# Optimization experiments

Hardware: AMD Instinct MI355X
Metric: run time of the kernel (lower is better)

The kernel has to match this reference:

```python
import jax, jax.numpy as jnp
import numpy as np

N, E, IN_C, HID, OUT_C = 50000, 800000, 128, 32, 32
EPS_BN = 1e-5


def gat_layer(x, src, dst, W, a_src, a_dst, bias, heads, out_c, concat):
    n = x.shape[0]
    h = (x @ W).reshape(n, heads, out_c)                    # [N,H,C]
    al_src = jnp.sum(h * a_src, axis=-1)                    # [N,H]
    al_dst = jnp.sum(h * a_dst, axis=-1)                    # [N,H]
    e = jax.nn.leaky_relu(al_src[src] + al_dst[dst], 0.2)   # [Etot,H]
    # segment softmax over incoming edges of each dst node
    m = jax.ops.segment_max(e, dst, num_segments=n)
    e = jnp.exp(e - jax.lax.stop_gradient(m)[dst])
    s = jax.ops.segment_sum(e, dst, num_segments=n)
    alpha = e / (s[dst] + 1e-16)                            # [Etot,H]
    msg = h[src] * alpha[..., None]                         # [Etot,H,C]
    out = jax.ops.segment_sum(msg, dst, num_segments=n)     # [N,H,C]
    out = out.reshape(n, heads * out_c) if concat else out.mean(axis=1)
    return out + bias


def bn_eval(x, w, b, m, v):
    return (x - m) * (w * jax.lax.rsqrt(v + EPS_BN)) + b


def setup_inputs() -> dict:
    key = jax.random.key(0)
    ks = jax.random.split(key, 12)
    f32 = jnp.float32
    inp = {
        'x': jax.random.normal(ks[0], (N, IN_C), dtype=f32),
        'edge_index': jax.random.randint(ks[1], (2, E), 0, N, dtype=jnp.int64),
        'w1': jax.random.normal(ks[2], (IN_C, 4 * HID), dtype=f32) * 0.1,
        'as1': jax.random.normal(ks[3], (4, HID), dtype=f32) * 0.1,
        'ad1': jax.random.normal(ks[4], (4, HID), dtype=f32) * 0.1,
        'b1': jnp.zeros((4 * HID,), f32),
        'bn1_w': jnp.ones((4 * HID,), f32), 'bn1_b': jnp.zeros((4 * HID,), f32),
        'bn1_m': jnp.zeros((4 * HID,), f32), 'bn1_v': jnp.ones((4 * HID,), f32),
        'w2': jax.random.normal(ks[5], (4 * HID, 4 * HID), dtype=f32) * 0.1,
        'as2': jax.random.normal(ks[6], (4, HID), dtype=f32) * 0.1,
        'ad2': jax.random.normal(ks[7], (4, HID), dtype=f32) * 0.1,
        'b2': jnp.zeros((4 * HID,), f32),
        'bn2_w': jnp.ones((4 * HID,), f32), 'bn2_b': jnp.zeros((4 * HID,), f32),
        'bn2_m': jnp.zeros((4 * HID,), f32), 'bn2_v': jnp.ones((4 * HID,), f32),
        'w3': jax.random.normal(ks[8], (4 * HID, OUT_C), dtype=f32) * 0.1,
        'as3': jax.random.normal(ks[9], (1, OUT_C), dtype=f32) * 0.1,
        'ad3': jax.random.normal(ks[10], (1, OUT_C), dtype=f32) * 0.1,
        'b3': jnp.zeros((OUT_C,), f32),
    }
    return inp


def reference(x, edge_index, w1, as1, ad1, b1, bn1_w, bn1_b, bn1_m, bn1_v,
              w2, as2, ad2, b2, bn2_w, bn2_b, bn2_m, bn2_v,
              w3, as3, ad3, b3):
    n = x.shape[0]
    loop = jnp.arange(n, dtype=edge_index.dtype)
    src = jnp.concatenate([edge_index[0], loop])  # add_self_loops (PyG default)
    dst = jnp.concatenate([edge_index[1], loop])
    # layer 1: GAT(heads=4, concat) -> BN(eval) -> relu (dropout=eval identity)
    h = gat_layer(x, src, dst, w1, as1, ad1, b1, 4, HID, True)
    h = jax.nn.relu(bn_eval(h, bn1_w, bn1_b, bn1_m, bn1_v))
    # layer 2
    h = gat_layer(h, src, dst, w2, as2, ad2, b2, 4, HID, True)
    h = jax.nn.relu(bn_eval(h, bn2_w, bn2_b, bn2_m, bn2_v))
    # layer 3: heads=1, concat=False
    return gat_layer(h, src, dst, w3, as3, ad3, b3, 1, OUT_C, False)
```

## Files before the change

### kernel.cpp

```cpp
#include <hip/hip_runtime.h>
#include <hip/hip_fp16.h>
#include <cstdint>


#define NBCHUNK 128
#define MAXBK 512

typedef _Float16 f16x8 __attribute__((ext_vector_type(8)));
typedef float f32x4 __attribute__((ext_vector_type(4)));

__device__ __forceinline__ float lrelu02(float x) {
  return x > 0.f ? x : 0.2f * x;
}

__device__ __forceinline__ float expw(float x) {
  return __expf(fminf(x, 80.f));
}

__global__ void detect_kernel(const unsigned* __restrict__ ei, int* __restrict__ flag) {
  int lane = threadIdx.x;
  unsigned w = ei[2 * lane + 1];
  unsigned long long nz = __ballot(w != 0u);
  if (lane == 0) *flag = (nz == 0ull) ? 1 : 0;
}

__global__ __launch_bounds__(256) void bcount_kernel(const void* __restrict__ ei, int E,
                                                     const int* __restrict__ flag,
                                                     int* __restrict__ counts,
                                                     int nbk, int chunk) {
  __shared__ int hist[MAXBK];
  for (int i = threadIdx.x; i < nbk; i += 256) hist[i] = 0;
  __syncthreads();
  int lo = blockIdx.x * chunk;
  int hi = lo + chunk; if (hi > E) hi = E;
  const bool is64 = (*flag) != 0;
  for (int e = lo + threadIdx.x; e < hi; e += 256) {
    int d = is64 ? (int)((const long long*)ei)[(size_t)E + e] : ((const int*)ei)[E + e];
    atomicAdd(&hist[d >> 7], 1);
  }
  __syncthreads();
  for (int i = threadIdx.x; i < nbk; i += 256)
    counts[(size_t)blockIdx.x * nbk + i] = hist[i];
}

__global__ void bscanT_kernel(int* __restrict__ counts, int* __restrict__ T, int nbk) {
  int b = blockIdx.x;
  int t = threadIdx.x;
  int lane = t & 63;
  int v = counts[(size_t)t * nbk + b];
  int inc = v;
#pragma unroll
  for (int off = 1; off < 64; off <<= 1) {
    int u = __shfl_up(inc, off);
    if (lane >= off) inc += u;
  }
  __shared__ int w0;
  if (t == 63) w0 = inc;
  __syncthreads();
  int wb = (t >= 64) ? w0 : 0;
  counts[(size_t)t * nbk + b] = wb + inc - v;
  if (t == 127) T[b] = wb + inc;
}

__global__ void bscanE_kernel(const int* __restrict__ T, int* __restrict__ EB, int nbk) {
  int lane = threadIdx.x;
  int carry = 0;
  for (int start = 0; start < nbk; start += 64) {
    int i = start + lane;
    int v = (i < nbk) ? T[i] : 0;
    int inc = v;
#pragma unroll
    for (int off = 1; off < 64; off <<= 1) {
      int u = __shfl_up(inc, off);
      if (lane >= off) inc += u;
    }
    if (i < nbk) EB[i] = inc - v + carry;
    carry += __shfl(inc, 63);
  }
  if (lane == 0) EB[nbk] = carry;
}

__global__ __launch_bounds__(256) void bemit_kernel(const void* __restrict__ ei, int E,
                                                    const int* __restrict__ flag,
                                                    const int* __restrict__ counts,
                                                    const int* __restrict__ EB,
                                                    int nbk, int chunk,
                                                    unsigned* __restrict__ binned) {
  __shared__ int cur[MAXBK];
  for (int i = threadIdx.x; i < nbk; i += 256)
    cur[i] = counts[(size_t)blockIdx.x * nbk + i] + EB[i];
  __syncthreads();
  int lo = blockIdx.x * chunk;
  int hi = lo + chunk; if (hi > E) hi = E;
  const bool is64 = (*flag) != 0;
  for (int e = lo + threadIdx.x; e < hi; e += 256) {
    int s, d;
    if (is64) {
      const long long* p = (const long long*)ei;
      s = (int)p[e];
      d = (int)p[(size_t)E + e];
    } else {
      const int* p = (const int*)ei;
      s = p[e];
      d = p[E + e];
    }
    int pos = atomicAdd(&cur[d >> 7], 1);
    binned[pos] = ((unsigned)(d & 127) << 16) | (unsigned)s;
  }
}

__global__ __launch_bounds__(256) void bscatter2_kernel(const unsigned* __restrict__ binned,
                                                        const int* __restrict__ EB,
                                                        int* __restrict__ row_ptr,
                                                        int* __restrict__ csr_src,
                                                        int n, int E) {
  __shared__ int hist[128];
  __shared__ int cur[128];
  __shared__ int w0s;
  const int b = blockIdx.x;
  const int t = threadIdx.x;
  const int bb = b << 7;
  if (t < 128) hist[t] = 0;
  __syncthreads();
  const int lo = EB[b], hi = EB[b + 1];
  for (int i = lo + t; i < hi; i += 256)
    atomicAdd(&hist[binned[i] >> 16], 1);
  __syncthreads();
  int lane = t & 63;
  int v = (t < 128) ? hist[t] : 0;
  int inc = v;
#pragma unroll
  for (int off = 1; off < 64; off <<= 1) {
    int u = __shfl_up(inc, off);
    if (lane >= off) inc += u;
  }
  if (t == 63) w0s = inc;
  __syncthreads();
  int exc = ((t >= 64 && t < 128) ? w0s : 0) + inc - v;
  if (t < 128 && bb + t < n) {
    int rp = EB[b] + bb + t + exc;
    row_ptr[bb + t] = rp;
    csr_src[rp] = bb + t;
    cur[t] = rp + 1;
  }
  if (b == 0 && t == 0) row_ptr[n] = E + n;
  __syncthreads();
  for (int i = lo + t; i < hi; i += 256) {
    unsigned pv = binned[i];
    int pos = atomicAdd(&cur[pv >> 16], 1);
    csr_src[pos] = (int)(pv & 0xFFFFu);
  }
}

__global__ void wcvt_kernel(const float* __restrict__ W, _Float16* __restrict__ Wt,
                            int OUTC) {
  int idx = blockIdx.x * 256 + threadIdx.x;
  if (idx >= 128 * OUTC) return;
  int k = idx / OUTC, c = idx % OUTC;
  Wt[(size_t)c * 128 + k] = (_Float16)W[idx];
}

template <int OUTC, int H, typename AT>
__global__ __launch_bounds__(256) void mfma_gemm_al_kernel(
    const AT* __restrict__ A, const _Float16* __restrict__ Wt,
    const float* __restrict__ a_src, const float* __restrict__ a_dst,
    __half* __restrict__ Hout, float* __restrict__ alS, float* __restrict__ alD,
    int n) {
  constexpr int NT = OUTC / 16;
  constexpr int APH = 136;

  __shared__ __align__(16) _Float16 A_lds[64 * APH];
  __shared__ __align__(16) _Float16 W_lds[OUTC * APH];

  const int t = threadIdx.x;
  const int r0 = blockIdx.x * 64;

  if constexpr (sizeof(AT) == 4) {
#pragma unroll
    for (int i = 0; i < 8; ++i) {
      int slot = t + i * 256;
      int r = slot >> 5, q = slot & 31;
      float4 v = make_float4(0.f, 0.f, 0.f, 0.f);
      if (r0 + r < n) v = *(const float4*)((const float*)A + (size_t)(r0 + r) * 128 + q * 4);
      __half2 p0 = __floats2half2_rn(v.x, v.y);
      __half2 p1 = __floats2half2_rn(v.z, v.w);
      uint2 pk;
      pk.x = *(unsigned*)&p0;
      pk.y = *(unsigned*)&p1;
      *(uint2*)&A_lds[r * APH + q * 4] = pk;
    }
  } else {
#pragma unroll
    for (int i = 0; i < 4; ++i) {
      int slot = t + i * 256;
      int r = slot >> 4, q = slot & 15;
      uint4 raw = make_uint4(0u, 0u, 0u, 0u);
      if (r0 + r < n) raw = *(const uint4*)((const __half*)A + (size_t)(r0 + r) * 128 + q * 8);
      *(uint4*)&A_lds[r * APH + q * 8] = raw;
    }
  }
#pragma unroll
  for (int i = 0; i < OUTC / 16; ++i) {
    int slot = t + i * 256;
    int c = slot >> 4, q = slot & 15;
    uint4 raw = *(const uint4*)(Wt + (size_t)c * 128 + q * 8);
    *(uint4*)&W_lds[c * APH + q * 8] = raw;
  }
  __syncthreads();

  const int w = t >> 6;
  const int lane = t & 63;
  const int lrow = lane & 15;
  const int lk = lane >> 4;

  f32x4 acc[NT];
#pragma unroll
  for (int i = 0; i < NT; ++i) acc[i] = (f32x4){0.f, 0.f, 0.f, 0.f};

#pragma unroll
  for (int kc = 0; kc < 4; ++kc) {
    f16x8 a = *(const f16x8*)&A_lds[(w * 16 + lrow) * APH + kc * 32 + lk * 8];
#pragma unroll
    for (int ct = 0; ct < NT; ++ct) {
      f16x8 b = *(const f16x8*)&W_lds[(ct * 16 + lrow) * APH + kc * 32 + lk * 8];
      acc[ct] = __builtin_amdgcn_mfma_f32_16x16x32_f16(a, b, acc[ct], 0, 0, 0);
    }
  }

  const int rbase = r0 + w * 16 + lk * 4;
#pragma unroll
  for (int ct = 0; ct < NT; ++ct) {
#pragma unroll
    for (int j = 0; j < 4; ++j) {
      int r = rbase + j;
      if (r < n) Hout[(size_t)r * OUTC + ct * 16 + lrow] = __float2half(acc[ct][j]);
    }
  }

#pragma unroll
  for (int h = 0; h < H; ++h) {
    float as0 = a_src[h * 32 + lrow], as1 = a_src[h * 32 + 16 + lrow];
    float ad0 = a_dst[h * 32 + lrow], ad1 = a_dst[h * 32 + 16 + lrow];
#pragma unroll
    for (int j = 0; j < 4; ++j) {
      float ps = acc[2 * h][j] * as0 + acc[2 * h + 1][j] * as1;
      float pd = acc[2 * h][j] * ad0 + acc[2 * h + 1][j] * ad1;
#pragma unroll
      for (int off = 1; off < 16; off <<= 1) {
        ps += __shfl_xor(ps, off);
        pd += __shfl_xor(pd, off);
      }
      if (lrow == 0) {
        int r = rbase + j;
        if (r < n) {
          alS[(size_t)r * H + h] = ps;
          alD[(size_t)r * H + h] = pd;
        }
      }
    }
  }
}

template <int H, bool BN, typename OutT>
__global__ __launch_bounds__(256) void agg_kernel(
    const int* __restrict__ row_ptr, const int* __restrict__ csr_src,
    const float* __restrict__ alS, const float* __restrict__ alD,
    const __half* __restrict__ hfeat, const float* __restrict__ bias,
    const float* __restrict__ bnw, const float* __restrict__ bnb,
    const float* __restrict__ bnm, const float* __restrict__ bnv,
    OutT* __restrict__ out, int n) {
  constexpr int LPN = (H == 4) ? 64 : 32;
  constexpr int NPB = 256 / LPN;
  constexpr int KCAP = 96;
  constexpr int RSH = (H == 4) ? 8 : 6;

  __shared__ __align__(16) float sW[NPB][KCAP * H];
  __shared__ int sOff[NPB][KCAP];

  const int slot = threadIdx.x / LPN;
  const int sl = threadIdx.x % LPN;
  const int v = blockIdx.x * NPB + slot;
  const bool active = v < n;
  const char* hb = (const char*)hfeat;

  int rs = 0, re = 0;
  if (active) { rs = row_ptr[v]; re = row_ptr[v + 1]; }
  const int deg = re - rs;
  const int degS = deg < KCAP ? deg : KCAP;

  if constexpr (H == 4) {
    float4 ad4 = make_float4(0.f, 0.f, 0.f, 0.f);
    if (active) ad4 = *(const float4*)(alD + (size_t)v * 4);
    float den0 = 0.f, den1 = 0.f, den2 = 0.f, den3 = 0.f;
    for (int k = sl; k < degS; k += 64) {
      int s = csr_src[rs + k];
      sOff[slot][k] = s << RSH;
      float4 a4 = *(const float4*)(alS + (size_t)s * 4);
      float u0 = expw(lrelu02(a4.x + ad4.x));
      float u1 = expw(lrelu02(a4.y + ad4.y));
      float u2 = expw(lrelu02(a4.z + ad4.z));
      float u3 = expw(lrelu02(a4.w + ad4.w));
      ((float4*)&sW[slot][0])[k] = make_float4(u0, u1, u2, u3);
      den0 += u0; den1 += u1; den2 += u2; den3 += u3;
    }
#pragma unroll
    for (int off = 32; off >= 1; off >>= 1) {
      den0 += __shfl_xor(den0, off);
      den1 += __shfl_xor(den1, off);
      den2 += __shfl_xor(den2, off);
      den3 += __shfl_xor(den3, off);
    }

    const int c = 2 * sl;
    const int h = sl >> 4;
    const unsigned cb2 = (unsigned)(c * 2);
    float2 acc = make_float2(0.f, 0.f);
    int j = 0;
    for (; j + 4 <= degS; j += 4) {
      unsigned o0 = (unsigned)sOff[slot][j + 0] + cb2;
      unsigned o1 = (unsigned)sOff[slot][j + 1] + cb2;
      unsigned o2 = (unsigned)sOff[slot][j + 2] + cb2;
      unsigned o3 = (unsigned)sOff[slot][j + 3] + cb2;
      float w0 = sW[slot][(j + 0) * 4 + h];
      float w1 = sW[slot][(j + 1) * 4 + h];
      float w2 = sW[slot][(j + 2) * 4 + h];
      float w3 = sW[slot][(j + 3) * 4 + h];
      float2 f0 = __half22float2(*(const __half2*)(hb + o0));
      float2 f1 = __half22float2(*(const __half2*)(hb + o1));
      float2 f2 = __half22float2(*(const __half2*)(hb + o2));
      float2 f3 = __half22float2(*(const __half2*)(hb + o3));
      acc.x = fmaf(w0, f0.x, acc.x); acc.y = fmaf(w0, f0.y, acc.y);
      acc.x = fmaf(w1, f1.x, acc.x); acc.y = fmaf(w1, f1.y, acc.y);
      acc.x = fmaf(w2, f2.x, acc.x); acc.y = fmaf(w2, f2.y, acc.y);
      acc.x = fmaf(w3, f3.x, acc.x); acc.y = fmaf(w3, f3.y, acc.y);
    }
    for (; j < degS; ++j) {
      unsigned o = (unsigned)sOff[slot][j] + cb2;
      float w = sW[slot][j * 4 + h];
      float2 f = __half22float2(*(const __half2*)(hb + o));
      acc.x = fmaf(w, f.x, acc.x); acc.y = fmaf(w, f.y, acc.y);
    }
    float den = (h == 0) ? den0 : (h == 1) ? den1 : (h == 2) ? den2 : den3;
    if (deg > KCAP) {
      float adh = alD[(size_t)v * 4 + h];
      for (int e = rs + KCAP; e < re; ++e) {
        int s = csr_src[e];
        float u = expw(lrelu02(alS[(size_t)s * 4 + h] + adh));
        den += u;
        float2 f = __half22float2(*(const __half2*)(hb + ((unsigned)(s << RSH) + cb2)));
        acc.x = fmaf(u, f.x, acc.x); acc.y = fmaf(u, f.y, acc.y);
      }
    }
    if (active) {
      float inv = 1.f / (den + 1e-16f);
      float2 b2v = *(const float2*)(bias + c);
      float g0 = acc.x * inv + b2v.x;
      float g1 = acc.y * inv + b2v.y;
      if constexpr (BN) {
        float2 bw = *(const float2*)(bnw + c);
        float2 bb = *(const float2*)(bnb + c);
        float2 bm = *(const float2*)(bnm + c);
        float2 bv = *(const float2*)(bnv + c);
        g0 = (g0 - bm.x) * (bw.x * rsqrtf(bv.x + 1e-5f)) + bb.x;
        g1 = (g1 - bm.y) * (bw.y * rsqrtf(bv.y + 1e-5f)) + bb.y;
        g0 = fmaxf(g0, 0.f);
        g1 = fmaxf(g1, 0.f);
      }
      if constexpr (sizeof(OutT) == 2) {
        __half2 o2 = __floats2half2_rn(g0, g1);
        *(__half2*)((__half*)out + (size_t)v * 128 + c) = o2;
      } else {
        *(float2*)((float*)out + (size_t)v * 128 + c) = make_float2(g0, g1);
      }
    }
  } else {
    float ad = active ? alD[v] : 0.f;
    float den = 0.f;
    for (int k = sl; k < degS; k += 32) {
      int s = csr_src[rs + k];
      sOff[slot][k] = s << RSH;
      float u = expw(lrelu02(alS[s] + ad));
      sW[slot][k] = u;
      den += u;
    }
#pragma unroll
    for (int off = 16; off >= 1; off >>= 1) den += __shfl_xor(den, off);

    const int c = sl;
    const unsigned cb2 = (unsigned)(c * 2);
    float acc = 0.f;
    int j = 0;
    for (; j + 4 <= degS; j += 4) {
      unsigned o0 = (unsigned)sOff[slot][j + 0] + cb2;
      unsigned o1 = (unsigned)sOff[slot][j + 1] + cb2;
      unsigned o2 = (unsigned)sOff[slot][j + 2] + cb2;
      unsigned o3 = (unsigned)sOff[slot][j + 3] + cb2;
      float w0 = sW[slot][j + 0], w1 = sW[slot][j + 1];
      float w2 = sW[slot][j + 2], w3 = sW[slot][j + 3];
      float f0 = __half2float(*(const __half*)(hb + o0));
      float f1 = __half2float(*(const __half*)(hb + o1));
      float f2 = __half2float(*(const __half*)(hb + o2));
      float f3 = __half2float(*(const __half*)(hb + o3));
      acc = fmaf(w0, f0, acc); acc = fmaf(w1, f1, acc);
      acc = fmaf(w2, f2, acc); acc = fmaf(w3, f3, acc);
    }
    for (; j < degS; ++j) {
      unsigned o = (unsigned)sOff[slot][j] + cb2;
      float w = sW[slot][j];
      acc = fmaf(w, __half2float(*(const __half*)(hb + o)), acc);
    }
    if (deg > KCAP) {
      for (int e = rs + KCAP; e < re; ++e) {
        int s = csr_src[e];
        float u = expw(lrelu02(alS[s] + ad));
        den += u;
        acc = fmaf(u, __half2float(*(const __half*)(hb + ((unsigned)(s << RSH) + cb2))), acc);
      }
    }
    if (active) {
      ((float*)out)[(size_t)v * 32 + c] = acc / (den + 1e-16f) + bias[c];
    }
  }
}

extern "C" void kernel_launch(void* const* d_in, const int* in_sizes, int n_in,
                              void* d_out, int out_size, void* d_ws, size_t ws_size,
                              hipStream_t stream) {
  const float* x = (const float*)d_in[0];
  const void* ei = d_in[1];
  const float* w1 = (const float*)d_in[2];
  const float* as1 = (const float*)d_in[3];
  const float* ad1 = (const float*)d_in[4];
  const float* b1 = (const float*)d_in[5];
  const float* bn1w = (const float*)d_in[6];
  const float* bn1b = (const float*)d_in[7];
  const float* bn1m = (const float*)d_in[8];
  const float* bn1v = (const float*)d_in[9];
  const float* w2 = (const float*)d_in[10];
  const float* as2 = (const float*)d_in[11];
  const float* ad2 = (const float*)d_in[12];
  const float* b2 = (const float*)d_in[13];
  const float* bn2w = (const float*)d_in[14];
  const float* bn2b = (const float*)d_in[15];
  const float* bn2m = (const float*)d_in[16];
  const float* bn2v = (const float*)d_in[17];
  const float* w3 = (const float*)d_in[18];
  const float* as3 = (const float*)d_in[19];
  const float* ad3 = (const float*)d_in[20];
  const float* b3 = (const float*)d_in[21];

  const int N = in_sizes[0] / 128;
  const int E = in_sizes[1] / 2;
  const int nbk = (N + 127) / 128;
  const int chunk = (E + NBCHUNK - 1) / NBCHUNK;

  char* base = (char*)d_ws;
  size_t off = 0;
  auto alloc = [&](size_t bytes) {
    void* p = base + off;
    off = (off + bytes + 255) & ~(size_t)255;
    return p;
  };
  int* flag = (int*)alloc(4);
  int* counts = (int*)alloc((size_t)NBCHUNK * nbk * 4);
  int* T = (int*)alloc((size_t)nbk * 4);
  int* EB = (int*)alloc((size_t)(nbk + 1) * 4);
  unsigned* binned = (unsigned*)alloc((size_t)E * 4);
  int* row_ptr = (int*)alloc((size_t)(N + 1) * 4);
  int* csr_src = (int*)alloc((size_t)(E + N) * 4);
  _Float16* Wt16 = (_Float16*)alloc((size_t)128 * 128 * 2);
  __half* hbuf = (__half*)alloc((size_t)N * 128 * 2);
  __half* gbuf = (__half*)alloc((size_t)N * 128 * 2);
  float* alS = (float*)alloc((size_t)N * 4 * 4);
  float* alD = (float*)alloc((size_t)N * 4 * 4);
  (void)ws_size;

  detect_kernel<<<1, 64, 0, stream>>>((const unsigned*)ei, flag);
  bcount_kernel<<<NBCHUNK, 256, 0, stream>>>(ei, E, flag, counts, nbk, chunk);
  bscanT_kernel<<<nbk, NBCHUNK, 0, stream>>>(counts, T, nbk);
  bscanE_kernel<<<1, 64, 0, stream>>>(T, EB, nbk);
  bemit_kernel<<<NBCHUNK, 256, 0, stream>>>(ei, E, flag, counts, EB, nbk, chunk, binned);
  bscatter2_kernel<<<nbk, 256, 0, stream>>>(binned, EB, row_ptr, csr_src, N, E);

  const int rowBlocks = (N + 63) / 64;

  wcvt_kernel<<<(128 * 128 + 255) / 256, 256, 0, stream>>>(w1, Wt16, 128);
  mfma_gemm_al_kernel<128, 4, float><<<rowBlocks, 256, 0, stream>>>(
      x, Wt16, as1, ad1, hbuf, alS, alD, N);
  agg_kernel<4, true, __half><<<(N + 3) / 4, 256, 0, stream>>>(
      row_ptr, csr_src, alS, alD, hbuf, b1, bn1w, bn1b, bn1m, bn1v, gbuf, N);
  wcvt_kernel<<<(128 * 128 + 255) / 256, 256, 0, stream>>>(w2, Wt16, 128);
  mfma_gemm_al_kernel<128, 4, __half><<<rowBlocks, 256, 0, stream>>>(
      gbuf, Wt16, as2, ad2, hbuf, alS, alD, N);
  agg_kernel<4, true, __half><<<(N + 3) / 4, 256, 0, stream>>>(
      row_ptr, csr_src, alS, alD, hbuf, b2, bn2w, bn2b, bn2m, bn2v, gbuf, N);
  wcvt_kernel<<<(128 * 32 + 255) / 256, 256, 0, stream>>>(w3, Wt16, 32);
  mfma_gemm_al_kernel<32, 1, __half><<<rowBlocks, 256, 0, stream>>>(
      gbuf, Wt16, as3, ad3, hbuf, alS, alD, N);
  agg_kernel<1, false, float><<<(N + 7) / 8, 256, 0, stream>>>(
      row_ptr, csr_src, alS, alD, hbuf, b3, nullptr, nullptr, nullptr, nullptr,
      (float*)d_out, N);
}
```

Baseline: 199.2 us.

## Widen aggregation gathers by splitting edges across half-waves, merge launch setup kernels

```diff
diff --git a/kernel.cpp b/kernel.cpp
--- a/kernel.cpp
+++ b/kernel.cpp
@@ -17,23 +17,24 @@
   return __expf(fminf(x, 80.f));
 }
 
-__global__ void detect_kernel(const unsigned* __restrict__ ei, int* __restrict__ flag) {
-  int lane = threadIdx.x;
-  unsigned w = ei[2 * lane + 1];
-  unsigned long long nz = __ballot(w != 0u);
-  if (lane == 0) *flag = (nz == 0ull) ? 1 : 0;
+__device__ __forceinline__ int detect64(const unsigned* ei) {
+  int is64 = 1;
+  for (int i = 1; i < 128; i += 2)
+    if (ei[i] != 0u) { is64 = 0; break; }
+  return is64;
 }
 
 __global__ __launch_bounds__(256) void bcount_kernel(const void* __restrict__ ei, int E,
-                                                     const int* __restrict__ flag,
                                                      int* __restrict__ counts,
                                                      int nbk, int chunk) {
   __shared__ int hist[MAXBK];
+  __shared__ int sIs64;
   for (int i = threadIdx.x; i < nbk; i += 256) hist[i] = 0;
+  if (threadIdx.x == 0) sIs64 = detect64((const unsigned*)ei);
   __syncthreads();
   int lo = blockIdx.x * chunk;
   int hi = lo + chunk; if (hi > E) hi = E;
-  const bool is64 = (*flag) != 0;
+  const bool is64 = sIs64 != 0;
   for (int e = lo + threadIdx.x; e < hi; e += 256) {
     int d = is64 ? (int)((const long long*)ei)[(size_t)E + e] : ((const int*)ei)[E + e];
     atomicAdd(&hist[d >> 7], 1);
@@ -81,18 +82,19 @@
 }
 
 __global__ __launch_bounds__(256) void bemit_kernel(const void* __restrict__ ei, int E,
-                                                    const int* __restrict__ flag,
                                                     const int* __restrict__ counts,
                                                     const int* __restrict__ EB,
                                                     int nbk, int chunk,
                                                     unsigned* __restrict__ binned) {
   __shared__ int cur[MAXBK];
+  __shared__ int sIs64;
   for (int i = threadIdx.x; i < nbk; i += 256)
     cur[i] = counts[(size_t)blockIdx.x * nbk + i] + EB[i];
+  if (threadIdx.x == 0) sIs64 = detect64((const unsigned*)ei);
   __syncthreads();
   int lo = blockIdx.x * chunk;
   int hi = lo + chunk; if (hi > E) hi = E;
-  const bool is64 = (*flag) != 0;
+  const bool is64 = sIs64 != 0;
   for (int e = lo + threadIdx.x; e < hi; e += 256) {
     int s, d;
     if (is64) {
@@ -152,12 +154,23 @@
   }
 }
 
-__global__ void wcvt_kernel(const float* __restrict__ W, _Float16* __restrict__ Wt,
-                            int OUTC) {
+__global__ void wcvt_all_kernel(const float* __restrict__ W1, const float* __restrict__ W2,
+                                const float* __restrict__ W3,
+                                _Float16* __restrict__ Wt1, _Float16* __restrict__ Wt2,
+                                _Float16* __restrict__ Wt3) {
   int idx = blockIdx.x * 256 + threadIdx.x;
-  if (idx >= 128 * OUTC) return;
-  int k = idx / OUTC, c = idx % OUTC;
-  Wt[(size_t)c * 128 + k] = (_Float16)W[idx];
+  if (idx < 16384) {
+    int k = idx >> 7, c = idx & 127;
+    Wt1[(size_t)c * 128 + k] = (_Float16)W1[idx];
+  } else if (idx < 32768) {
+    int i = idx - 16384;
+    int k = i >> 7, c = i & 127;
+    Wt2[(size_t)c * 128 + k] = (_Float16)W2[i];
+  } else if (idx < 36864) {
+    int i = idx - 32768;
+    int k = i >> 5, c = i & 31;
+    Wt3[(size_t)c * 128 + k] = (_Float16)W3[i];
+  }
 }
 
 template <int OUTC, int H, typename AT>
@@ -311,66 +324,114 @@
       den3 += __shfl_xor(den3, off);
     }
 
-    const int c = 2 * sl;
-    const int h = sl >> 4;
+    const int half = sl >> 5;
+    const int l5 = sl & 31;
+    const int c = l5 * 4;
+    const int h = l5 >> 3;
     const unsigned cb2 = (unsigned)(c * 2);
-    float2 acc = make_float2(0.f, 0.f);
+    float a0 = 0.f, a1 = 0.f, a2 = 0.f, a3 = 0.f;
     int j = 0;
-    for (; j + 4 <= degS; j += 4) {
-      unsigned o0 = (unsigned)sOff[slot][j + 0] + cb2;
-      unsigned o1 = (unsigned)sOff[slot][j + 1] + cb2;
-      unsigned o2 = (unsigned)sOff[slot][j + 2] + cb2;
-      unsigned o3 = (unsigned)sOff[slot][j + 3] + cb2;
-      float w0 = sW[slot][(j + 0) * 4 + h];
-      float w1 = sW[slot][(j + 1) * 4 + h];
-      float w2 = sW[slot][(j + 2) * 4 + h];
-      float w3 = sW[slot][(j + 3) * 4 + h];
-      float2 f0 = __half22float2(*(const __half2*)(hb + o0));
-      float2 f1 = __half22float2(*(const __half2*)(hb + o1));
-      float2 f2 = __half22float2(*(const __half2*)(hb + o2));
-      float2 f3 = __half22float2(*(const __half2*)(hb + o3));
-      acc.x = fmaf(w0, f0.x, acc.x); acc.y = fmaf(w0, f0.y, acc.y);
-      acc.x = fmaf(w1, f1.x, acc.x); acc.y = fmaf(w1, f1.y, acc.y);
-      acc.x = fmaf(w2, f2.x, acc.x); acc.y = fmaf(w2, f2.y, acc.y);
-      acc.x = fmaf(w3, f3.x, acc.x); acc.y = fmaf(w3, f3.y, acc.y);
-    }
-    for (; j < degS; ++j) {
-      unsigned o = (unsigned)sOff[slot][j] + cb2;
-      float w = sW[slot][j * 4 + h];
-      float2 f = __half22float2(*(const __half2*)(hb + o));
-      acc.x = fmaf(w, f.x, acc.x); acc.y = fmaf(w, f.y, acc.y);
-    }
+    for (; j + 8 <= degS; j += 8) {
+      int e0 = j + half, e1 = j + 2 + half, e2 = j + 4 + half, e3 = j + 6 + half;
+      unsigned o0 = (unsigned)sOff[slot][e0] + cb2;
+      unsigned o1 = (unsigned)sOff[slot][e1] + cb2;
+      unsigned o2 = (unsigned)sOff[slot][e2] + cb2;
+      unsigned o3 = (unsigned)sOff[slot][e3] + cb2;
+      float w0 = sW[slot][e0 * 4 + h], w1 = sW[slot][e1 * 4 + h];
+      float w2 = sW[slot][e2 * 4 + h], w3 = sW[slot][e3 * 4 + h];
+      uint2 r0v = *(const uint2*)(hb + o0);
+      uint2 r1v = *(const uint2*)(hb + o1);
+      uint2 r2v = *(const uint2*)(hb + o2);
+      uint2 r3v = *(const uint2*)(hb + o3);
+      float2 f0l = __half22float2(*(const __half2*)&r0v.x);
+      float2 f0h = __half22float2(*(const __half2*)&r0v.y);
+      float2 f1l = __half22float2(*(const __half2*)&r1v.x);
+      float2 f1h = __half22float2(*(const __half2*)&r1v.y);
+      float2 f2l = __half22float2(*(const __half2*)&r2v.x);
+      float2 f2h = __half22float2(*(const __half2*)&r2v.y);
+      float2 f3l = __half22float2(*(const __half2*)&r3v.x);
+      float2 f3h = __half22float2(*(const __half2*)&r3v.y);
+      a0 = fmaf(w0, f0l.x, a0); a1 = fmaf(w0, f0l.y, a1);
+      a2 = fmaf(w0, f0h.x, a2); a3 = fmaf(w0, f0h.y, a3);
+      a0 = fmaf(w1, f1l.x, a0); a1 = fmaf(w1, f1l.y, a1);
+      a2 = fmaf(w1, f1h.x, a2); a3 = fmaf(w1, f1h.y, a3);
+      a0 = fmaf(w2, f2l.x, a0); a1 = fmaf(w2, f2l.y, a1);
+      a2 = fmaf(w2, f2h.x, a2); a3 = fmaf(w2, f2h.y, a3);
+      a0 = fmaf(w3, f3l.x, a0); a1 = fmaf(w3, f3l.y, a1);
+      a2 = fmaf(w3, f3h.x, a2); a3 = fmaf(w3, f3h.y, a3);
+    }
+    for (; j + 2 <= degS; j += 2) {
+      int e = j + half;
+      unsigned o = (unsigned)sOff[slot][e] + cb2;
+      float w = sW[slot][e * 4 + h];
+      uint2 rv = *(const uint2*)(hb + o);
+      float2 fl = __half22float2(*(const __half2*)&rv.x);
+      float2 fh = __half22float2(*(const __half2*)&rv.y);
+      a0 = fmaf(w, fl.x, a0); a1 = fmaf(w, fl.y, a1);
+      a2 = fmaf(w, fh.x, a2); a3 = fmaf(w, fh.y, a3);
+    }
+    if ((degS & 1) && half == 0) {
+      int e = degS - 1;
+      unsigned o = (unsigned)sOff[slot][e] + cb2;
+      float w = sW[slot][e * 4 + h];
+      uint2 rv = *(const uint2*)(hb + o);
+      float2 fl = __half22float2(*(const __half2*)&rv.x);
+      float2 fh = __half22float2(*(const __half2*)&rv.y);
+      a0 = fmaf(w, fl.x, a0); a1 = fmaf(w, fl.y, a1);
+      a2 = fmaf(w, fh.x, a2); a3 = fmaf(w, fh.y, a3);
+    }
+    a0 += __shfl_xor(a0, 32);
+    a1 += __shfl_xor(a1, 32);
+    a2 += __shfl_xor(a2, 32);
+    a3 += __shfl_xor(a3, 32);
+
     float den = (h == 0) ? den0 : (h == 1) ? den1 : (h == 2) ? den2 : den3;
     if (deg > KCAP) {
       float adh = alD[(size_t)v * 4 + h];
-      for (int e = rs + KCAP; e < re; ++e) {
-        int s = csr_src[e];
-        float u = expw(lrelu02(alS[(size_t)s * 4 + h] + adh));
-        den += u;
-        float2 f = __half22float2(*(const __half2*)(hb + ((unsigned)(s << RSH) + cb2)));
-        acc.x = fmaf(u, f.x, acc.x); acc.y = fmaf(u, f.y, acc.y);
+      if (half == 0) {
+        for (int e = rs + KCAP; e < re; ++e) {
+          int s = csr_src[e];
+          float u = expw(lrelu02(alS[(size_t)s * 4 + h] + adh));
+          den += u;
+          uint2 rv = *(const uint2*)(hb + ((unsigned)(s << RSH) + cb2));
+          float2 fl = __half22float2(*(const __half2*)&rv.x);
+          float2 fh = __half22float2(*(const __half2*)&rv.y);
+          a0 = fmaf(u, fl.x, a0); a1 = fmaf(u, fl.y, a1);
+          a2 = fmaf(u, fh.x, a2); a3 = fmaf(u, fh.y, a3);
+        }
+      } else {
+        for (int e = rs + KCAP; e < re; ++e) {
+          int s = csr_src[e];
+          den += expw(lrelu02(alS[(size_t)s * 4 + h] + adh));
+        }
       }
     }
-    if (active) {
+    if (active && half == 0) {
       float inv = 1.f / (den + 1e-16f);
-      float2 b2v = *(const float2*)(bias + c);
-      float g0 = acc.x * inv + b2v.x;
-      float g1 = acc.y * inv + b2v.y;
+      float4 b4 = *(const float4*)(bias + c);
+      float g0 = a0 * inv + b4.x;
+      float g1 = a1 * inv + b4.y;
+      float g2 = a2 * inv + b4.z;
+      float g3 = a3 * inv + b4.w;
       if constexpr (BN) {
-        float2 bw = *(const float2*)(bnw + c);
-        float2 bb = *(const float2*)(bnb + c);
-        float2 bm = *(const float2*)(bnm + c);
-        float2 bv = *(const float2*)(bnv + c);
-        g0 = (g0 - bm.x) * (bw.x * rsqrtf(bv.x + 1e-5f)) + bb.x;
-        g1 = (g1 - bm.y) * (bw.y * rsqrtf(bv.y + 1e-5f)) + bb.y;
-        g0 = fmaxf(g0, 0.f);
-        g1 = fmaxf(g1, 0.f);
+        float4 bw = *(const float4*)(bnw + c);
+        float4 bb = *(const float4*)(bnb + c);
+        float4 bm = *(const float4*)(bnm + c);
+        float4 bv = *(const float4*)(bnv + c);
+        g0 = fmaxf((g0 - bm.x) * (bw.x * rsqrtf(bv.x + 1e-5f)) + bb.x, 0.f);
+        g1 = fmaxf((g1 - bm.y) * (bw.y * rsqrtf(bv.y + 1e-5f)) + bb.y, 0.f);
+        g2 = fmaxf((g2 - bm.z) * (bw.z * rsqrtf(bv.z + 1e-5f)) + bb.z, 0.f);
+        g3 = fmaxf((g3 - bm.w) * (bw.w * rsqrtf(bv.w + 1e-5f)) + bb.w, 0.f);
       }
       if constexpr (sizeof(OutT) == 2) {
-        __half2 o2 = __floats2half2_rn(g0, g1);
-        *(__half2*)((__half*)out + (size_t)v * 128 + c) = o2;
+        __half2 p0 = __floats2half2_rn(g0, g1);
+        __half2 p1 = __floats2half2_rn(g2, g3);
+        uint2 pk;
+        pk.x = *(unsigned*)&p0;
+        pk.y = *(unsigned*)&p1;
+        *(uint2*)((__half*)out + (size_t)v * 128 + c) = pk;
       } else {
-        *(float2*)((float*)out + (size_t)v * 128 + c) = make_float2(g0, g1);
+        *(float4*)((float*)out + (size_t)v * 128 + c) = make_float4(g0, g1, g2, g3);
       }
     }
   } else {
@@ -386,39 +447,58 @@
 #pragma unroll
     for (int off = 16; off >= 1; off >>= 1) den += __shfl_xor(den, off);
 
-    const int c = sl;
-    const unsigned cb2 = (unsigned)(c * 2);
-    float acc = 0.f;
+    const int quad = sl >> 4;
+    const int l4 = sl & 15;
+    const int c2 = l4 * 2;
+    const unsigned cb2 = (unsigned)(c2 * 2);
+    float a0 = 0.f, a1 = 0.f;
     int j = 0;
     for (; j + 4 <= degS; j += 4) {
-      unsigned o0 = (unsigned)sOff[slot][j + 0] + cb2;
-      unsigned o1 = (unsigned)sOff[slot][j + 1] + cb2;
-      unsigned o2 = (unsigned)sOff[slot][j + 2] + cb2;
-      unsigned o3 = (unsigned)sOff[slot][j + 3] + cb2;
-      float w0 = sW[slot][j + 0], w1 = sW[slot][j + 1];
-      float w2 = sW[slot][j + 2], w3 = sW[slot][j + 3];
-      float f0 = __half2float(*(const __half*)(hb + o0));
-      float f1 = __half2float(*(const __half*)(hb + o1));
-      float f2 = __half2float(*(const __half*)(hb + o2));
-      float f3 = __half2float(*(const __half*)(hb + o3));
-      acc = fmaf(w0, f0, acc); acc = fmaf(w1, f1, acc);
-      acc = fmaf(w2, f2, acc); acc = fmaf(w3, f3, acc);
-    }
-    for (; j < degS; ++j) {
-      unsigned o = (unsigned)sOff[slot][j] + cb2;
-      float w = sW[slot][j];
-      acc = fmaf(w, __half2float(*(const __half*)(hb + o)), acc);
-    }
+      int e0 = j + quad, e1 = j + 2 + quad;
+      unsigned o0 = (unsigned)sOff[slot][e0] + cb2;
+      unsigned o1 = (unsigned)sOff[slot][e1] + cb2;
+      float w0 = sW[slot][e0], w1 = sW[slot][e1];
+      float2 f0 = __half22float2(*(const __half2*)(hb + o0));
+      float2 f1 = __half22float2(*(const __half2*)(hb + o1));
+      a0 = fmaf(w0, f0.x, a0); a1 = fmaf(w0, f0.y, a1);
+      a0 = fmaf(w1, f1.x, a0); a1 = fmaf(w1, f1.y, a1);
+    }
+    for (; j + 2 <= degS; j += 2) {
+      int e = j + quad;
+      unsigned o = (unsigned)sOff[slot][e] + cb2;
+      float w = sW[slot][e];
+      float2 f = __half22float2(*(const __half2*)(hb + o));
+      a0 = fmaf(w, f.x, a0); a1 = fmaf(w, f.y, a1);
+    }
+    if ((degS & 1) && quad == 0) {
+      int e = degS - 1;
+      unsigned o = (unsigned)sOff[slot][e] + cb2;
+      float w = sW[slot][e];
+      float2 f = __half22float2(*(const __half2*)(hb + o));
+      a0 = fmaf(w, f.x, a0); a1 = fmaf(w, f.y, a1);
+    }
+    a0 += __shfl_xor(a0, 16);
+    a1 += __shfl_xor(a1, 16);
+
     if (deg > KCAP) {
-      for (int e = rs + KCAP; e < re; ++e) {
-        int s = csr_src[e];
-        float u = expw(lrelu02(alS[s] + ad));
-        den += u;
-        acc = fmaf(u, __half2float(*(const __half*)(hb + ((unsigned)(s << RSH) + cb2))), acc);
+      if (quad == 0) {
+        for (int e = rs + KCAP; e < re; ++e) {
+          int s = csr_src[e];
+          float u = expw(lrelu02(alS[s] + ad));
+          den += u;
+          float2 f = __half22float2(*(const __half2*)(hb + ((unsigned)(s << RSH) + cb2)));
+          a0 = fmaf(u, f.x, a0); a1 = fmaf(u, f.y, a1);
+        }
+      } else {
+        for (int e = rs + KCAP; e < re; ++e)
+          den += expw(lrelu02(alS[csr_src[e]] + ad));
       }
     }
-    if (active) {
-      ((float*)out)[(size_t)v * 32 + c] = acc / (den + 1e-16f) + bias[c];
+    if (active && quad == 0) {
+      float inv = 1.f / (den + 1e-16f);
+      float2 b2v = *(const float2*)(bias + c2);
+      ((float2*)((float*)out + (size_t)v * 32))[l4] =
+          make_float2(a0 * inv + b2v.x, a1 * inv + b2v.y);
     }
   }
 }
@@ -461,42 +541,40 @@
     off = (off + bytes + 255) & ~(size_t)255;
     return p;
   };
-  int* flag = (int*)alloc(4);
   int* counts = (int*)alloc((size_t)NBCHUNK * nbk * 4);
   int* T = (int*)alloc((size_t)nbk * 4);
   int* EB = (int*)alloc((size_t)(nbk + 1) * 4);
   unsigned* binned = (unsigned*)alloc((size_t)E * 4);
   int* row_ptr = (int*)alloc((size_t)(N + 1) * 4);
   int* csr_src = (int*)alloc((size_t)(E + N) * 4);
-  _Float16* Wt16 = (_Float16*)alloc((size_t)128 * 128 * 2);
+  _Float16* Wt1 = (_Float16*)alloc((size_t)128 * 128 * 2);
+  _Float16* Wt2 = (_Float16*)alloc((size_t)128 * 128 * 2);
+  _Float16* Wt3 = (_Float16*)alloc((size_t)32 * 128 * 2);
   __half* hbuf = (__half*)alloc((size_t)N * 128 * 2);
   __half* gbuf = (__half*)alloc((size_t)N * 128 * 2);
   float* alS = (float*)alloc((size_t)N * 4 * 4);
   float* alD = (float*)alloc((size_t)N * 4 * 4);
   (void)ws_size;
 
-  detect_kernel<<<1, 64, 0, stream>>>((const unsigned*)ei, flag);
-  bcount_kernel<<<NBCHUNK, 256, 0, stream>>>(ei, E, flag, counts, nbk, chunk);
+  wcvt_all_kernel<<<144, 256, 0, stream>>>(w1, w2, w3, Wt1, Wt2, Wt3);
+  bcount_kernel<<<NBCHUNK, 256, 0, stream>>>(ei, E, counts, nbk, chunk);
   bscanT_kernel<<<nbk, NBCHUNK, 0, stream>>>(counts, T, nbk);
   bscanE_kernel<<<1, 64, 0, stream>>>(T, EB, nbk);
-  bemit_kernel<<<NBCHUNK, 256, 0, stream>>>(ei, E, flag, counts, EB, nbk, chunk, binned);
+  bemit_kernel<<<NBCHUNK, 256, 0, stream>>>(ei, E, counts, EB, nbk, chunk, binned);
   bscatter2_kernel<<<nbk, 256, 0, stream>>>(binned, EB, row_ptr, csr_src, N, E);
 
   const int rowBlocks = (N + 63) / 64;
 
-  wcvt_kernel<<<(128 * 128 + 255) / 256, 256, 0, stream>>>(w1, Wt16, 128);
   mfma_gemm_al_kernel<128, 4, float><<<rowBlocks, 256, 0, stream>>>(
-      x, Wt16, as1, ad1, hbuf, alS, alD, N);
+      x, Wt1, as1, ad1, hbuf, alS, alD, N);
   agg_kernel<4, true, __half><<<(N + 3) / 4, 256, 0, stream>>>(
       row_ptr, csr_src, alS, alD, hbuf, b1, bn1w, bn1b, bn1m, bn1v, gbuf, N);
-  wcvt_kernel<<<(128 * 128 + 255) / 256, 256, 0, stream>>>(w2, Wt16, 128);
   mfma_gemm_al_kernel<128, 4, __half><<<rowBlocks, 256, 0, stream>>>(
-      gbuf, Wt16, as2, ad2, hbuf, alS, alD, N);
+      gbuf, Wt2, as2, ad2, hbuf, alS, alD, N);
   agg_kernel<4, true, __half><<<(N + 3) / 4, 256, 0, stream>>>(
       row_ptr, csr_src, alS, alD, hbuf, b2, bn2w, bn2b, bn2m, bn2v, gbuf, N);
-  wcvt_kernel<<<(128 * 32 + 255) / 256, 256, 0, stream>>>(w3, Wt16, 32);
   mfma_gemm_al_kernel<32, 1, __half><<<rowBlocks, 256, 0, stream>>>(
-      gbuf, Wt16, as3, ad3, hbuf, alS, alD, N);
+      gbuf, Wt3, as3, ad3, hbuf, alS, alD, N);
   agg_kernel<1, false, float><<<(N + 7) / 8, 256, 0, stream>>>(
       row_ptr, csr_src, alS, alD, hbuf, b3, nullptr, nullptr, nullptr, nullptr,
       (float*)d_out, N);
```

After: 192.0 us. 3.6% less time.
